# Performance work log

Measured on AMD Instinct MI355X. Metric: run time of the kernel, lower is better.

## Reference

```python
import jax, jax.numpy as jnp
import numpy as np

N_PP = 8192      # number of papers (nodes_num_pp)
N_A = 8192       # number of authors
N_AP = N_PP + N_A  # nodes_num_ap (stacked paper+author id space)
DIM = 16
E = 262144
ALPHA = 0.5


def _cdist(x, y):
    # Euclidean cdist via Gram trick; avoids (B, A, D) broadcast intermediate.
    x2 = jnp.sum(x * x, axis=-1)[:, None]
    y2 = jnp.sum(y * y, axis=-1)[None, :]
    d2 = x2 + y2 - 2.0 * (x @ y.T)
    return jnp.sqrt(jnp.maximum(d2, 0.0))


def setup_inputs() -> dict:
    key = jax.random.key(0)
    ks = jax.random.split(key, 8)
    p_star = jax.random.normal(ks[0], (N_PP, DIM), dtype=jnp.float32)
    p = jax.random.normal(ks[1], (N_PP, DIM), dtype=jnp.float32)
    a = jax.random.normal(ks[2], (N_A, DIM), dtype=jnp.float32)
    beta_ap = 2.0 * jax.random.uniform(ks[3], (N_AP,), dtype=jnp.float32) - 1.0
    gamma_pp = 2.0 * jax.random.uniform(ks[4], (2 * N_PP,), dtype=jnp.float32) - 1.0
    edges_pp = jax.random.randint(ks[5], (2, E), 0, N_PP)
    e_ap0 = jax.random.randint(ks[6], (E,), 0, N_PP)
    e_ap1 = jax.random.randint(ks[7], (E,), N_PP, N_AP)
    edges_ap = jnp.stack([e_ap0, e_ap1])
    p_star_nodes = jnp.arange(N_PP, dtype=jnp.int32)
    p_nodes = jnp.arange(N_PP, dtype=jnp.int32)
    a_nodes = jnp.arange(N_A, dtype=jnp.int32) + N_PP
    return {"p_star": p_star, "p": p, "a": a, "beta_ap": beta_ap,
            "gamma_pp": gamma_pp, "edges_pp": edges_pp, "edges_ap": edges_ap,
            "p_star_nodes": p_star_nodes, "p_nodes": p_nodes, "a_nodes": a_nodes}


def reference(p_star, p, a, beta_ap, gamma_pp, edges_pp, edges_ap,
              p_star_nodes, p_nodes, a_nodes):
    # ---------- paper-paper (pp) term ----------
    ps_sel = p_star[p_star_nodes]                    # (B, D)
    p_sel = p[p_nodes]                               # (P, D)
    g_ps = gamma_pp[p_star_nodes]                    # (B,)
    g_p = gamma_pp[p_nodes + N_PP]                   # (P,)
    # gamma_mat.T - dist_mat, shape (B, P)
    m_pp = jnp.exp(g_ps[:, None] + g_p[None, :] - _cdist(ps_sel, p_sel))
    nonlink_pp = jnp.sum(jnp.triu(m_pp, k=1))        # strict upper triangle
    gamma_pair = gamma_pp[edges_pp[0]] + gamma_pp[edges_pp[1] + N_PP]
    d_pp = jnp.linalg.norm(p_star[edges_pp[0]] - p[edges_pp[1]], axis=-1)
    link_pp = jnp.sum(gamma_pair - d_pp)
    nll_pp = -(link_pp - nonlink_pp)

    # ---------- author-paper (ap) term ----------
    a_sel = a[a_nodes - N_PP]                        # (A, D)
    b_ps = beta_ap[p_star_nodes]                     # (B,)
    b_a = beta_ap[a_nodes]                           # (A,)
    # intended math: beta_mat.T - dist_mat, shape (B, A)
    m_ap = jnp.exp(b_ps[:, None] + b_a[None, :] - _cdist(ps_sel, a_sel))
    nonlink_ap = jnp.sum(m_ap)
    beta_pair = beta_ap[edges_ap[0]] + beta_ap[edges_ap[1]]
    d_ap = jnp.linalg.norm(p_star[edges_ap[0]] - a[edges_ap[1] - N_PP], axis=-1)
    link_ap = jnp.sum(beta_pair - d_ap)
    nll_ap = -(link_ap - nonlink_ap)

    n_p = p_nodes.shape[0]
    n_a = a_nodes.shape[0]
    return ALPHA * nll_pp / n_p + (1.0 - ALPHA) * nll_ap / n_a
```

## Files before the change

kernel.cpp:

```cpp
#include <hip/hip_runtime.h>
#include <stdint.h>

#define N_PP   8192
#define DIM    16
#define NEDGE  262144
#define LOG2E  1.4426950408889634f

#define WS_EDGE  8
#define WS_PSBF  512
#define WS_PBF   (WS_PSBF + 65536)
#define WS_ABF   (WS_PBF  + 65536)
#define WS_X2PS  (WS_ABF  + 65536)
#define WS_Y2P   (WS_X2PS + 8192)
#define WS_Y2A   (WS_Y2P  + 8192)
#define WS_EGC   (WS_Y2A  + 8192)
#define WS_EBC   (WS_EGC  + 8192)
#define WS_GL2   (WS_EBC  + 8192)
#define WS_BL2   (WS_GL2  + 8192)

#define NQ_AP  1024
#define NQ_PP  544
#define NB_MAT (NQ_AP + NQ_PP)

typedef short    bf16x8 __attribute__((ext_vector_type(8)));
typedef float    f32x4  __attribute__((ext_vector_type(4)));
typedef unsigned u32x4  __attribute__((ext_vector_type(4)));

__device__ __forceinline__ float waveReduce(float v) {
#pragma unroll
    for (int off = 32; off > 0; off >>= 1)
        v += __shfl_down(v, off, 64);
    return v;
}

__device__ __forceinline__ unsigned bf16_rne(float f) {
    unsigned u = __builtin_bit_cast(unsigned, f);
    return (u + 0x7FFFu + ((u >> 16) & 1u)) >> 16;
}
__device__ __forceinline__ unsigned packbf2(float a, float b) {
    return bf16_rne(a) | (bf16_rne(b) << 16);
}

__device__ __forceinline__ void gload_lds(const uint32_t* g, uint32_t* l) {
    __builtin_amdgcn_global_load_lds(
        (const __attribute__((address_space(1))) void*)(uintptr_t)g,
        (__attribute__((address_space(3))) void*)(unsigned)(uintptr_t)l,
        16, 0, 0);
}

__global__ __launch_bounds__(256) void pre_kernel(
    const float* __restrict__ p_star, const float* __restrict__ p,
    const float* __restrict__ a, const float* __restrict__ beta_ap,
    const float* __restrict__ gamma_pp, const int* __restrict__ edges_pp,
    const int* __restrict__ edges_ap, float* __restrict__ ws)
{
    const int b = blockIdx.x, tid = threadIdx.x;

    if (b < 224) {
        const int g = b * 256 + tid;
        if (g < 8) ws[g] = 0.0f;
        if (g < 3 * 8192) {
            const int arr = g >> 13, idx = g & 8191;
            const float* src = arr == 0 ? p_star : (arr == 1 ? p : a);
            const int bfo = arr == 0 ? WS_PSBF : (arr == 1 ? WS_PBF : WS_ABF);
            const int n2o = arr == 0 ? WS_X2PS : (arr == 1 ? WS_Y2P : WS_Y2A);
            const float4* rp = (const float4*)(src + idx * DIM);
            float4 f0 = rp[0], f1 = rp[1], f2 = rp[2], f3 = rp[3];
            float n2 = f0.x*f0.x + f0.y*f0.y + f0.z*f0.z + f0.w*f0.w
                     + f1.x*f1.x + f1.y*f1.y + f1.z*f1.z + f1.w*f1.w
                     + f2.x*f2.x + f2.y*f2.y + f2.z*f2.z + f2.w*f2.w
                     + f3.x*f3.x + f3.y*f3.y + f3.z*f3.z + f3.w*f3.w;
            u32x4 u0 = { packbf2(f0.x, f0.y), packbf2(f0.z, f0.w),
                         packbf2(f1.x, f1.y), packbf2(f1.z, f1.w) };
            u32x4 u1 = { packbf2(f2.x, f2.y), packbf2(f2.z, f2.w),
                         packbf2(f3.x, f3.y), packbf2(f3.z, f3.w) };
            u32x4* dst = (u32x4*)(ws + bfo) + idx * 2;
            dst[0] = u0; dst[1] = u1;
            ws[n2o + idx] = n2;
        } else if (g < 7 * 8192) {
            const int h = g - 3 * 8192, q = h >> 13, i = h & 8191;
            if      (q == 0) ws[WS_EGC + i] = __expf(gamma_pp[8192 + i]);
            else if (q == 1) ws[WS_EBC + i] = __expf(beta_ap[8192 + i]);
            else if (q == 2) ws[WS_GL2 + i] = gamma_pp[i] * LOG2E;
            else             ws[WS_BL2 + i] = beta_ap[i] * LOG2E;
        }
    } else {
        __shared__ float smred[4];
        const int  eb   = b - 224;
        const bool isPP = (eb < 128);
        const int  base = (isPP ? eb : eb - 128) * 2048;
        float sum = 0.f;
#pragma unroll
        for (int k = 0; k < 8; ++k) {
            const int e = base + k * 256 + tid;
            const float* yrow;
            float bias;
            int e0;
            if (isPP) {
                e0 = edges_pp[e];
                int e1 = edges_pp[NEDGE + e];
                yrow = p + e1 * DIM;
                bias = gamma_pp[e0] + gamma_pp[N_PP + e1];
            } else {
                e0 = edges_ap[e];
                int e1 = edges_ap[NEDGE + e];
                yrow = a + (e1 - N_PP) * DIM;
                bias = beta_ap[e0] + beta_ap[e1];
            }
            const float4* xp = (const float4*)(p_star + e0 * DIM);
            const float4* yp = (const float4*)yrow;
            float d2 = 0.f;
#pragma unroll
            for (int kk = 0; kk < 4; ++kk) {
                float4 xv = xp[kk], yv = yp[kk];
                float dx = xv.x - yv.x, dy = xv.y - yv.y,
                      dz = xv.z - yv.z, dw = xv.w - yv.w;
                d2 += dx*dx + dy*dy + dz*dz + dw*dw;
            }
            sum += bias - __builtin_amdgcn_sqrtf(d2);
        }
        float wsum = waveReduce(sum);
        if ((tid & 63) == 0) smred[tid >> 6] = wsum;
        __syncthreads();
        if (tid == 0)
            ws[WS_EDGE + eb] = smred[0] + smred[1] + smred[2] + smred[3];
    }
}

__global__ void main_kernel(float* __restrict__ ws, float* __restrict__ out)
{
    __shared__ uint32_t sbuf[5120];
    const int b = blockIdx.x, tid = threadIdx.x, wid = tid >> 6;
    const int lane = tid & 63, quad = lane >> 4, l16 = lane & 15;

    const bool isPP = (b >= NQ_AP);
    int g, c;
    if (!isPP) { g = b >> 4; c = b & 15; }
    else {
        const int qq = b - NQ_AP;
        int bnd = 0;
        while (2 * (bnd + 1) * (bnd + 2) <= qq) ++bnd;
        const int r = qq - 2 * bnd * (bnd + 1);
        g = 4 * bnd + r / (bnd + 1);
        c = r % (bnd + 1);
    }
    const int t0 = c << 5;

    const uint32_t* Xbf = (const uint32_t*)(ws + WS_PSBF);
    const uint32_t* Ybf = (const uint32_t*)(ws + (isPP ? WS_PBF : WS_ABF));
    const float* x2a = ws + WS_X2PS;
    const float* y2  = ws + (isPP ? WS_Y2P : WS_Y2A);
    const float* gl2 = ws + (isPP ? WS_GL2 : WS_BL2);
    const float* EcA = ws + (isPP ? WS_EGC : WS_EBC);

    const int sA = (g << 3) + (wid << 1);
    bf16x8 bfrag[2];
    float  y2c[2], Ec[2];
#pragma unroll
    for (int ss = 0; ss < 2; ++ss) {
        const int j = ((sA + ss) << 4) + l16;
        u32x4 bu = {0u, 0u, 0u, 0u};
        if (quad < 2) bu = *(const u32x4*)(Ybf + j * 8 + (quad << 2));
        bfrag[ss] = __builtin_bit_cast(bf16x8, bu);
        y2c[ss] = y2[j];
        Ec[ss]  = EcA[j];
    }

    for (int k = wid; k < 20; k += 4) {
        const uint32_t* gsrc;
        int loff;
        if (k < 16)      { gsrc = Xbf + (t0 << 7) + (k << 8);            loff = k << 8; }
        else if (k < 18) { gsrc = (const uint32_t*)(x2a + (t0 << 4)) + ((k - 16) << 8);
                           loff = 4096 + ((k - 16) << 8); }
        else             { gsrc = (const uint32_t*)(gl2 + (t0 << 4)) + ((k - 18) << 8);
                           loff = 4608 + ((k - 18) << 8); }
        gload_lds(gsrc + (lane << 2), &sbuf[loff]);
    }
    __syncthreads();

    const f32x4 zero4 = {0.f, 0.f, 0.f, 0.f};
    float acc[2] = {0.f, 0.f};
    const int tHi = isPP ? (sA + 1 < t0 + 32 ? sA + 2 : t0 + 32) : t0 + 32;
    for (int t = t0; t < tHi; ++t) {
        const int tl = t - t0;
        const u32x4 au = *(const u32x4*)&sbuf[(tl << 7) + (l16 << 3) + ((quad & 1) << 2)];
        const f32x4 x24 = *(const f32x4*)((const float*)sbuf + 4096 + (tl << 4) + (quad << 2));
        const f32x4 ag4 = *(const f32x4*)((const float*)sbuf + 4608 + (tl << 4) + (quad << 2));
#pragma unroll
        for (int ss = 0; ss < 2; ++ss) {
            const int s = sA + ss;
            if (isPP && t > s) continue;
            f32x4 d = __builtin_amdgcn_mfma_f32_16x16x32_bf16(
                __builtin_bit_cast(bf16x8, au), bfrag[ss], zero4, 0, 0, 0);
            if (!isPP || t < s) {
#pragma unroll
                for (int r = 0; r < 4; ++r) {
                    float d2 = fmaf(-2.f, d[r], x24[r] + y2c[ss]);
                    d2 = fmaxf(d2, 0.f);
                    acc[ss] += __builtin_amdgcn_exp2f(
                        fmaf(-LOG2E, __builtin_amdgcn_sqrtf(d2), ag4[r]));
                }
            } else {
#pragma unroll
                for (int r = 0; r < 4; ++r) {
                    float d2 = fmaf(-2.f, d[r], x24[r] + y2c[ss]);
                    d2 = fmaxf(d2, 0.f);
                    float term = __builtin_amdgcn_exp2f(
                        fmaf(-LOG2E, __builtin_amdgcn_sqrtf(d2), ag4[r]));
                    if (l16 <= (quad << 2) + r) term = 0.f;
                    acc[ss] += term;
                }
            }
        }
    }
    const float val = acc[0] * Ec[0] + acc[1] * Ec[1];

    const float wsum = waveReduce(val);
    __syncthreads();
    float* smred = (float*)sbuf;
    if (lane == 0) smred[wid] = wsum;
    __syncthreads();
    if (tid == 0) {
        atomicAdd(&ws[isPP ? 2 : 0], smred[0] + smred[1] + smred[2] + smred[3]);
        __threadfence();
        unsigned old = atomicAdd((unsigned*)(ws + 4), 1u);
        if (old == NB_MAT - 1) {
            float s0 = atomicAdd(&ws[0], 0.f);
            float s2 = atomicAdd(&ws[2], 0.f);
            float lpp = 0.f, lap = 0.f;
            for (int i = 0; i < 128; i += 4) {
                const float4 v = *(const float4*)(ws + WS_EDGE + i);
                const float4 u = *(const float4*)(ws + WS_EDGE + 128 + i);
                lpp += v.x + v.y + v.z + v.w;
                lap += u.x + u.y + u.z + u.w;
            }
            out[0] = 0.5f * (s0 - lpp) / (float)N_PP
                   + 0.5f * (s2 - lap) / (float)N_PP;
        }
    }
}

extern "C" void kernel_launch(void* const* d_in, const int* in_sizes, int n_in,
                              void* d_out, int out_size, void* d_ws, size_t ws_size,
                              hipStream_t stream) {
    const float* p_star   = (const float*)d_in[0];
    const float* p        = (const float*)d_in[1];
    const float* a        = (const float*)d_in[2];
    const float* beta_ap  = (const float*)d_in[3];
    const float* gamma_pp = (const float*)d_in[4];
    const int*   edges_pp = (const int*)d_in[5];
    const int*   edges_ap = (const int*)d_in[6];

    float* ws  = (float*)d_ws;
    float* out = (float*)d_out;

    hipLaunchKernelGGL(pre_kernel, dim3(480), dim3(256), 0, stream,
                       p_star, p, a, beta_ap, gamma_pp, edges_pp, edges_ap, ws);
    hipLaunchKernelGGL(main_kernel, dim3(NB_MAT), dim3(256), 0, stream, ws, out);
}
```

Baseline: 139.1 us.

## Convert main kernel to persistent blocks pulling half-size tiles from atomic queue

```diff
diff --git a/kernel.cpp b/kernel.cpp
--- a/kernel.cpp
+++ b/kernel.cpp
@@ -18,9 +18,10 @@
 #define WS_GL2   (WS_EBC  + 8192)
 #define WS_BL2   (WS_GL2  + 8192)
 
-#define NQ_AP  1024
-#define NQ_PP  544
-#define NB_MAT (NQ_AP + NQ_PP)
+#define NQ_AP2  2048
+#define NQ_PP2  1056
+#define NQ_TOT  (NQ_AP2 + NQ_PP2)
+#define NB_PERS 2048
 
 typedef short    bf16x8 __attribute__((ext_vector_type(8)));
 typedef float    f32x4  __attribute__((ext_vector_type(4)));
@@ -127,104 +128,118 @@
     }
 }
 
-__global__ void main_kernel(float* __restrict__ ws, float* __restrict__ out)
+__global__ __launch_bounds__(256) void main_kernel(
+    float* __restrict__ ws, float* __restrict__ out)
 {
-    __shared__ uint32_t sbuf[5120];
-    const int b = blockIdx.x, tid = threadIdx.x, wid = tid >> 6;
+    __shared__ uint32_t sbuf[2560];
+    __shared__ float smred[8];
+    __shared__ unsigned qsh;
+    const int tid = threadIdx.x, wid = tid >> 6;
     const int lane = tid & 63, quad = lane >> 4, l16 = lane & 15;
 
-    const bool isPP = (b >= NQ_AP);
-    int g, c;
-    if (!isPP) { g = b >> 4; c = b & 15; }
-    else {
-        const int qq = b - NQ_AP;
-        int bnd = 0;
-        while (2 * (bnd + 1) * (bnd + 2) <= qq) ++bnd;
-        const int r = qq - 2 * bnd * (bnd + 1);
-        g = 4 * bnd + r / (bnd + 1);
-        c = r % (bnd + 1);
+    const uint32_t* Xbf = (const uint32_t*)(ws + WS_PSBF);
+    const float* x2a = ws + WS_X2PS;
+    const f32x4 zero4 = {0.f, 0.f, 0.f, 0.f};
+
+    float accPP = 0.f, accAP = 0.f;
+
+    for (;;) {
+        __syncthreads();
+        if (tid == 0) qsh = atomicAdd((unsigned*)(ws + 5), 1u);
+        __syncthreads();
+        const unsigned q = qsh;
+        if (q >= NQ_TOT) break;
+
+        const bool isPP = (q >= NQ_AP2);
+        int g, c;
+        if (!isPP) { g = q >> 5; c = q & 31; }
+        else {
+            const int qq = q - NQ_AP2;
+            int m = 0;
+            while ((m + 1) * (m + 2) <= qq) ++m;
+            const int r = qq - m * (m + 1);
+            g = 2 * m + r / (m + 1);
+            c = r % (m + 1);
+        }
+        const int t0 = c << 4;
+
+        const uint32_t* Ybf = (const uint32_t*)(ws + (isPP ? WS_PBF : WS_ABF));
+        const float* y2  = ws + (isPP ? WS_Y2P : WS_Y2A);
+        const float* gl2 = ws + (isPP ? WS_GL2 : WS_BL2);
+        const float* EcA = ws + (isPP ? WS_EGC : WS_EBC);
+
+        const int sA = (g << 3) + (wid << 1);
+        bf16x8 bfrag[2];
+        float  y2c[2], Ec[2];
+#pragma unroll
+        for (int ss = 0; ss < 2; ++ss) {
+            const int j = ((sA + ss) << 4) + l16;
+            u32x4 bu = {0u, 0u, 0u, 0u};
+            if (quad < 2) bu = *(const u32x4*)(Ybf + j * 8 + (quad << 2));
+            bfrag[ss] = __builtin_bit_cast(bf16x8, bu);
+            y2c[ss] = y2[j];
+            Ec[ss]  = EcA[j];
+        }
+
+        for (int k = wid; k < 10; k += 4) {
+            const uint32_t* gsrc;
+            int loff;
+            if (k < 8)       { gsrc = Xbf + (c << 11) + (k << 8); loff = k << 8; }
+            else if (k == 8) { gsrc = (const uint32_t*)(x2a + (c << 8)); loff = 2048; }
+            else             { gsrc = (const uint32_t*)(gl2 + (c << 8)); loff = 2304; }
+            gload_lds(gsrc + (lane << 2), &sbuf[loff]);
+        }
+        __syncthreads();
+
+        float acc[2] = {0.f, 0.f};
+        const int tEnd = t0 + 16;
+        const int tHi  = isPP ? (sA + 2 < tEnd ? sA + 2 : tEnd) : tEnd;
+        for (int t = t0; t < tHi; ++t) {
+            const int tl = t - t0;
+            const u32x4 au = *(const u32x4*)&sbuf[(tl << 7) + (l16 << 3) + ((quad & 1) << 2)];
+            const f32x4 x24 = *(const f32x4*)((const float*)sbuf + 2048 + (tl << 4) + (quad << 2));
+            const f32x4 ag4 = *(const f32x4*)((const float*)sbuf + 2304 + (tl << 4) + (quad << 2));
+#pragma unroll
+            for (int ss = 0; ss < 2; ++ss) {
+                const int s = sA + ss;
+                if (isPP && t > s) continue;
+                f32x4 d = __builtin_amdgcn_mfma_f32_16x16x32_bf16(
+                    __builtin_bit_cast(bf16x8, au), bfrag[ss], zero4, 0, 0, 0);
+                if (!isPP || t < s) {
+#pragma unroll
+                    for (int r = 0; r < 4; ++r) {
+                        float d2 = fmaf(-2.f, d[r], x24[r] + y2c[ss]);
+                        d2 = fmaxf(d2, 0.f);
+                        acc[ss] += __builtin_amdgcn_exp2f(
+                            fmaf(-LOG2E, __builtin_amdgcn_sqrtf(d2), ag4[r]));
+                    }
+                } else {
+#pragma unroll
+                    for (int r = 0; r < 4; ++r) {
+                        float d2 = fmaf(-2.f, d[r], x24[r] + y2c[ss]);
+                        d2 = fmaxf(d2, 0.f);
+                        float term = __builtin_amdgcn_exp2f(
+                            fmaf(-LOG2E, __builtin_amdgcn_sqrtf(d2), ag4[r]));
+                        if (l16 <= (quad << 2) + r) term = 0.f;
+                        acc[ss] += term;
+                    }
+                }
+            }
+        }
+        const float v = acc[0] * Ec[0] + acc[1] * Ec[1];
+        if (isPP) accPP += v; else accAP += v;
     }
-    const int t0 = c << 5;
-
-    const uint32_t* Xbf = (const uint32_t*)(ws + WS_PSBF);
-    const uint32_t* Ybf = (const uint32_t*)(ws + (isPP ? WS_PBF : WS_ABF));
-    const float* x2a = ws + WS_X2PS;
-    const float* y2  = ws + (isPP ? WS_Y2P : WS_Y2A);
-    const float* gl2 = ws + (isPP ? WS_GL2 : WS_BL2);
-    const float* EcA = ws + (isPP ? WS_EGC : WS_EBC);
-
-    const int sA = (g << 3) + (wid << 1);
-    bf16x8 bfrag[2];
-    float  y2c[2], Ec[2];
-#pragma unroll
-    for (int ss = 0; ss < 2; ++ss) {
-        const int j = ((sA + ss) << 4) + l16;
-        u32x4 bu = {0u, 0u, 0u, 0u};
-        if (quad < 2) bu = *(const u32x4*)(Ybf + j * 8 + (quad << 2));
-        bfrag[ss] = __builtin_bit_cast(bf16x8, bu);
-        y2c[ss] = y2[j];
-        Ec[ss]  = EcA[j];
-    }
-
-    for (int k = wid; k < 20; k += 4) {
-        const uint32_t* gsrc;
-        int loff;
-        if (k < 16)      { gsrc = Xbf + (t0 << 7) + (k << 8);            loff = k << 8; }
-        else if (k < 18) { gsrc = (const uint32_t*)(x2a + (t0 << 4)) + ((k - 16) << 8);
-                           loff = 4096 + ((k - 16) << 8); }
-        else             { gsrc = (const uint32_t*)(gl2 + (t0 << 4)) + ((k - 18) << 8);
-                           loff = 4608 + ((k - 18) << 8); }
-        gload_lds(gsrc + (lane << 2), &sbuf[loff]);
-    }
-    __syncthreads();
-
-    const f32x4 zero4 = {0.f, 0.f, 0.f, 0.f};
-    float acc[2] = {0.f, 0.f};
-    const int tHi = isPP ? (sA + 1 < t0 + 32 ? sA + 2 : t0 + 32) : t0 + 32;
-    for (int t = t0; t < tHi; ++t) {
-        const int tl = t - t0;
-        const u32x4 au = *(const u32x4*)&sbuf[(tl << 7) + (l16 << 3) + ((quad & 1) << 2)];
-        const f32x4 x24 = *(const f32x4*)((const float*)sbuf + 4096 + (tl << 4) + (quad << 2));
-        const f32x4 ag4 = *(const f32x4*)((const float*)sbuf + 4608 + (tl << 4) + (quad << 2));
-#pragma unroll
-        for (int ss = 0; ss < 2; ++ss) {
-            const int s = sA + ss;
-            if (isPP && t > s) continue;
-            f32x4 d = __builtin_amdgcn_mfma_f32_16x16x32_bf16(
-                __builtin_bit_cast(bf16x8, au), bfrag[ss], zero4, 0, 0, 0);
-            if (!isPP || t < s) {
-#pragma unroll
-                for (int r = 0; r < 4; ++r) {
-                    float d2 = fmaf(-2.f, d[r], x24[r] + y2c[ss]);
-                    d2 = fmaxf(d2, 0.f);
-                    acc[ss] += __builtin_amdgcn_exp2f(
-                        fmaf(-LOG2E, __builtin_amdgcn_sqrtf(d2), ag4[r]));
-                }
-            } else {
-#pragma unroll
-                for (int r = 0; r < 4; ++r) {
-                    float d2 = fmaf(-2.f, d[r], x24[r] + y2c[ss]);
-                    d2 = fmaxf(d2, 0.f);
-                    float term = __builtin_amdgcn_exp2f(
-                        fmaf(-LOG2E, __builtin_amdgcn_sqrtf(d2), ag4[r]));
-                    if (l16 <= (quad << 2) + r) term = 0.f;
-                    acc[ss] += term;
-                }
-            }
-        }
-    }
-    const float val = acc[0] * Ec[0] + acc[1] * Ec[1];
-
-    const float wsum = waveReduce(val);
-    __syncthreads();
-    float* smred = (float*)sbuf;
-    if (lane == 0) smred[wid] = wsum;
+
+    const float wPP = waveReduce(accPP);
+    const float wAP = waveReduce(accAP);
+    if (lane == 0) { smred[wid] = wPP; smred[4 + wid] = wAP; }
     __syncthreads();
     if (tid == 0) {
-        atomicAdd(&ws[isPP ? 2 : 0], smred[0] + smred[1] + smred[2] + smred[3]);
+        atomicAdd(&ws[0], smred[0] + smred[1] + smred[2] + smred[3]);
+        atomicAdd(&ws[2], smred[4] + smred[5] + smred[6] + smred[7]);
         __threadfence();
         unsigned old = atomicAdd((unsigned*)(ws + 4), 1u);
-        if (old == NB_MAT - 1) {
+        if (old == NB_PERS - 1) {
             float s0 = atomicAdd(&ws[0], 0.f);
             float s2 = atomicAdd(&ws[2], 0.f);
             float lpp = 0.f, lap = 0.f;
@@ -256,5 +271,5 @@
 
     hipLaunchKernelGGL(pre_kernel, dim3(480), dim3(256), 0, stream,
                        p_star, p, a, beta_ap, gamma_pp, edges_pp, edges_ap, ws);
-    hipLaunchKernelGGL(main_kernel, dim3(NB_MAT), dim3(256), 0, stream, ws, out);
-}
+    hipLaunchKernelGGL(main_kernel, dim3(NB_PERS), dim3(256), 0, stream, ws, out);
+}
```

Measured after the change: 226.9 us. 1.63x slower.
